# Kernel tuning notes

Hardware: AMD Instinct MI355X
Metric: run time of the kernel (lower is better)

The kernel has to match this reference:

```python
import jax, jax.numpy as jnp
import numpy as np

DIM = 64  # scaling dim from __init__


def setup_inputs() -> dict:
    key = jax.random.key(0)
    kq, kk, kv = jax.random.split(key, 3)
    B, N, D = 16, 2048, 64
    Q = jax.random.normal(kq, (B, N, D), dtype=jnp.float32)
    K = jax.random.normal(kk, (B, N, D), dtype=jnp.float32)
    V = jax.random.normal(kv, (B, N, D), dtype=jnp.float32)
    return {"Q": Q, "K": K, "V": V}


def reference(Q, K, V):
    # Original transposes K to [B, d, N]; the E/F Linformer projections are
    # constructed but their application guards are always False, so the math
    # is plain scaled-dot-product attention. Dropout p=0 (eval baseline).
    scale = 1.0 / (DIM ** 0.5)
    QK = jnp.einsum('bnd,bmd->bnm', Q, K) * scale          # [B, N, N]
    attn_weights = jax.nn.softmax(QK, axis=-1)             # [B, N, N]
    out = jnp.einsum('bnm,bmd->bnd', attn_weights, V)      # [B, N, d]
    return out, attn_weights
```

## Files before the change

### kernel.cpp

```cpp
#include <hip/hip_runtime.h>
#include <hip/hip_bf16.h>

#define B_  16
#define N_  2048
#define D_  64
#define SCALE_LOG2 0.18033688011112042f

typedef __attribute__((ext_vector_type(8))) short  frag8;
typedef __attribute__((ext_vector_type(4))) float  floatx4;

union FragU { frag8 fr; unsigned short us[8]; };

__device__ __forceinline__ unsigned short f2bf(float f) {
    return __builtin_bit_cast(unsigned short, __float2bfloat16(f));
}
__device__ __forceinline__ float exp2fast(float x) {
    return __builtin_amdgcn_exp2f(x);
}

__global__ __launch_bounds__(256) void denom_kernel(
    const float* __restrict__ Q, const float* __restrict__ K,
    float* __restrict__ ws)
{
    __shared__ unsigned short Ks[64][72];

    const int id    = blockIdx.x;
    const int xcd   = id & 7;
    const int s     = id >> 3;
    const int b     = xcd * 2 + (s >> 7);
    const int rem   = s & 127;
    const int qtile = rem >> 2;
    const int kq    = rem & 3;
    const int qbase = qtile * 64;
    const int kbase = kq * 512;
    const size_t bN = (size_t)b * N_;

    const int tid  = threadIdx.x;
    const int w    = tid >> 6;
    const int lane = tid & 63;
    const int lm   = lane & 15;
    const int quad = lane >> 4;
    const int q8   = quad * 8;
    const int srow = tid >> 2;
    const int sc0  = (tid & 3) * 16;

    FragU aq0, aq1;
    {
        const float* qp = Q + (bN + qbase + w*16 + lm) * D_;
        float4 f0 = *(const float4*)(qp + q8);
        float4 f1 = *(const float4*)(qp + q8 + 4);
        float4 f2 = *(const float4*)(qp + 32 + q8);
        float4 f3 = *(const float4*)(qp + 36 + q8);
        #pragma unroll
        for (int j = 0; j < 4; ++j) {
            aq0.us[j]   = f2bf(f0[j]);  aq0.us[4+j] = f2bf(f1[j]);
            aq1.us[j]   = f2bf(f2[j]);  aq1.us[4+j] = f2bf(f3[j]);
        }
    }

    float s4[4] = {0.f, 0.f, 0.f, 0.f};

    ushort4 kreg[4];
    {
        const float4* src = (const float4*)(K + (bN + kbase + srow) * D_ + sc0);
        #pragma unroll
        for (int i = 0; i < 4; ++i) {
            float4 f = src[i];
            kreg[i].x=f2bf(f.x); kreg[i].y=f2bf(f.y);
            kreg[i].z=f2bf(f.z); kreg[i].w=f2bf(f.w);
        }
    }

    for (int t = 0; t < 8; ++t) {
        __syncthreads();
        #pragma unroll
        for (int i = 0; i < 4; ++i)
            *(ushort4*)&Ks[srow][sc0 + i*4] = kreg[i];
        __syncthreads();

        float4 fnext[4];
        if (t + 1 < 8) {
            const float4* src = (const float4*)(K + (bN + kbase + (t+1)*64 + srow) * D_ + sc0);
            #pragma unroll
            for (int i = 0; i < 4; ++i) fnext[i] = src[i];
        }

        __builtin_amdgcn_s_setprio(1);
        #pragma unroll
        for (int ns = 0; ns < 4; ++ns) {
            frag8 b0 = *(const frag8*)&Ks[ns*16 + lm][q8];
            frag8 b1 = *(const frag8*)&Ks[ns*16 + lm][32 + q8];
            floatx4 a = {0.f, 0.f, 0.f, 0.f};
            a = __builtin_amdgcn_mfma_f32_16x16x32_bf16(aq0.fr, b0, a, 0, 0, 0);
            a = __builtin_amdgcn_mfma_f32_16x16x32_bf16(aq1.fr, b1, a, 0, 0, 0);
            #pragma unroll
            for (int r = 0; r < 4; ++r)
                s4[r] += exp2fast(a[r] * SCALE_LOG2);
        }
        __builtin_amdgcn_s_setprio(0);

        if (t + 1 < 8) {
            #pragma unroll
            for (int i = 0; i < 4; ++i) {
                kreg[i].x=f2bf(fnext[i].x); kreg[i].y=f2bf(fnext[i].y);
                kreg[i].z=f2bf(fnext[i].z); kreg[i].w=f2bf(fnext[i].w);
            }
        }
    }

    #pragma unroll
    for (int r = 0; r < 4; ++r) {
        float v = s4[r];
        #pragma unroll
        for (int off = 1; off < 16; off <<= 1)
            v += __shfl_xor(v, off, 64);
        if (lm == 0)
            atomicAdd(&ws[bN + qbase + w*16 + quad*4 + r], v);
    }
}

struct __align__(16) SMemB {
    unsigned short Ks[64][72];
    unsigned short Vt[64][72];
    float          Pf[4][16][68];
};

__global__ __launch_bounds__(256, 4) void attn_kernel(
    const float* __restrict__ Q, const float* __restrict__ K,
    const float* __restrict__ V, const float* __restrict__ ws,
    float* __restrict__ out, float* __restrict__ attn)
{
    __shared__ SMemB sm;

    const int id    = blockIdx.x;
    const int xcd   = id & 7;
    const int s     = id >> 3;
    const int b     = xcd * 2 + (s >> 6);
    const int rem   = s & 63;
    const int qtile = rem >> 1;
    const int kh    = rem & 1;
    const int qbase = qtile * 64;
    const int kbase = kh * 1024;
    const size_t bN = (size_t)b * N_;

    const int tid  = threadIdx.x;
    const int w    = tid >> 6;
    const int lane = tid & 63;
    const int lm   = lane & 15;
    const int quad = lane >> 4;
    const int q8   = quad * 8;
    const int srow = tid >> 2;
    const int sc0  = (tid & 3) * 16;
    const int vswz = srow ^ (((sc0 >> 4) & 3) << 3);

    FragU aq0, aq1;
    {
        const float* qp = Q + (bN + qbase + w*16 + lm) * D_;
        float4 f0 = *(const float4*)(qp + q8);
        float4 f1 = *(const float4*)(qp + q8 + 4);
        float4 f2 = *(const float4*)(qp + 32 + q8);
        float4 f3 = *(const float4*)(qp + 36 + q8);
        #pragma unroll
        for (int j = 0; j < 4; ++j) {
            aq0.us[j]   = f2bf(f0[j]);  aq0.us[4+j] = f2bf(f1[j]);
            aq1.us[j]   = f2bf(f2[j]);  aq1.us[4+j] = f2bf(f3[j]);
        }
    }

    float invl[4];
    #pragma unroll
    for (int r = 0; r < 4; ++r)
        invl[r] = 1.0f / ws[bN + qbase + w*16 + quad*4 + r];

    floatx4 oacc[4];
    #pragma unroll
    for (int dg = 0; dg < 4; ++dg) oacc[dg] = (floatx4){0.f, 0.f, 0.f, 0.f};

    const int prow = lane >> 3;
    const int pcol = (lane & 7) * 4;

    float4 fk[4], fv[4];
    auto loadS = [&](int t) {
        const float4* srcK = (const float4*)(K + (bN + kbase + t*64 + srow) * D_ + sc0);
        const float4* srcV = (const float4*)(V + (bN + kbase + t*64 + srow) * D_ + sc0);
        #pragma unroll
        for (int i = 0; i < 4; ++i) fk[i] = srcK[i];
        #pragma unroll
        for (int i = 0; i < 4; ++i) fv[i] = srcV[i];
    };

    loadS(0);
    for (int t = 0; t < 16; ++t) {
        __syncthreads();
        #pragma unroll
        for (int i = 0; i < 4; ++i) {
            ushort4 u; u.x=f2bf(fk[i].x); u.y=f2bf(fk[i].y);
                       u.z=f2bf(fk[i].z); u.w=f2bf(fk[i].w);
            *(ushort4*)&sm.Ks[srow][sc0 + i*4] = u;
        }
        #pragma unroll
        for (int i = 0; i < 4; ++i) {
            sm.Vt[sc0 + i*4 + 0][vswz] = f2bf(fv[i].x);
            sm.Vt[sc0 + i*4 + 1][vswz] = f2bf(fv[i].y);
            sm.Vt[sc0 + i*4 + 2][vswz] = f2bf(fv[i].z);
            sm.Vt[sc0 + i*4 + 3][vswz] = f2bf(fv[i].w);
        }
        __syncthreads();

        if (t + 1 < 16) loadS(t + 1);

        floatx4 acc[4];
        __builtin_amdgcn_s_setprio(1);
        #pragma unroll
        for (int ns = 0; ns < 4; ++ns) {
            frag8 b0 = *(const frag8*)&sm.Ks[ns*16 + lm][q8];
            frag8 b1 = *(const frag8*)&sm.Ks[ns*16 + lm][32 + q8];
            floatx4 a = {0.f, 0.f, 0.f, 0.f};
            a = __builtin_amdgcn_mfma_f32_16x16x32_bf16(aq0.fr, b0, a, 0, 0, 0);
            a = __builtin_amdgcn_mfma_f32_16x16x32_bf16(aq1.fr, b1, a, 0, 0, 0);
            acc[ns] = a;
        }
        __builtin_amdgcn_s_setprio(0);

        #pragma unroll
        for (int ns = 0; ns < 4; ++ns)
            #pragma unroll
            for (int r = 0; r < 4; ++r)
                sm.Pf[w][quad*4 + r][ns*16 + lm] =
                    exp2fast(acc[ns][r] * SCALE_LOG2) * invl[r];

        #pragma unroll
        for (int rg = 0; rg < 2; ++rg)
            #pragma unroll
            for (int half = 0; half < 2; ++half) {
                floatx4 pv = *(const floatx4*)&sm.Pf[w][rg*8 + prow][half*32 + pcol];
                __builtin_nontemporal_store(pv,
                    (floatx4*)&attn[(bN + qbase + w*16 + rg*8 + prow) * N_
                                    + kbase + t*64 + half*32 + pcol]);
            }

        FragU pa0, pa1;
        {
            float4 p0 = *(const float4*)&sm.Pf[w][lm][q8];
            float4 p1 = *(const float4*)&sm.Pf[w][lm][q8 + 4];
            float4 p2 = *(const float4*)&sm.Pf[w][lm][32 + q8];
            float4 p3 = *(const float4*)&sm.Pf[w][lm][36 + q8];
            #pragma unroll
            for (int j = 0; j < 4; ++j) {
                pa0.us[j]   = f2bf(p0[j]);  pa0.us[4+j] = f2bf(p1[j]);
                pa1.us[j]   = f2bf(p2[j]);  pa1.us[4+j] = f2bf(p3[j]);
            }
        }

        __builtin_amdgcn_s_setprio(1);
        #pragma unroll
        for (int dg = 0; dg < 4; ++dg) {
            const int kb = q8 ^ (dg << 3);
            frag8 v0 = *(const frag8*)&sm.Vt[dg*16 + lm][kb];
            frag8 v1 = *(const frag8*)&sm.Vt[dg*16 + lm][32 + kb];
            oacc[dg] = __builtin_amdgcn_mfma_f32_16x16x32_bf16(pa0.fr, v0, oacc[dg], 0, 0, 0);
            oacc[dg] = __builtin_amdgcn_mfma_f32_16x16x32_bf16(pa1.fr, v1, oacc[dg], 0, 0, 0);
        }
        __builtin_amdgcn_s_setprio(0);
    }

    #pragma unroll
    for (int dg = 0; dg < 4; ++dg)
        #pragma unroll
        for (int r = 0; r < 4; ++r)
            atomicAdd(&out[(bN + qbase + w*16 + quad*4 + r) * D_ + dg*16 + lm],
                      oacc[dg][r]);
}

extern "C" void kernel_launch(void* const* d_in, const int* in_sizes, int n_in,
                              void* d_out, int out_size, void* d_ws, size_t ws_size,
                              hipStream_t stream) {
    const float* Q = (const float*)d_in[0];
    const float* K = (const float*)d_in[1];
    const float* V = (const float*)d_in[2];
    float* out  = (float*)d_out;
    float* attn = out + (size_t)B_ * N_ * D_;
    float* ws   = (float*)d_ws;

    hipMemsetAsync(ws, 0, (size_t)B_ * N_ * sizeof(float), stream);
    hipMemsetAsync(out, 0, (size_t)B_ * N_ * D_ * sizeof(float), stream);
    denom_kernel<<<dim3(2048), 256, 0, stream>>>(Q, K, ws);
    attn_kernel <<<dim3(1024), 256, 0, stream>>>(Q, K, V, ws, out, attn);
}
```

Before: 363.1 us.

## Store unnormalized bf16 P transposed in LDS and write attn directly

Replaces the fp32 P staging buffer in shared memory with a smaller transposed bf16 buffer of unnormalized probabilities. The PV A-fragments are then gathered from it with scalar 16-bit reads, and the 1/l normalization moves to the final output atomics. Attention weights are now written straight from registers with scalar stores rather than vectorized nontemporal float4 stores through LDS. This cuts LDS footprint and traffic, but risks less efficient global store coalescing and many small LDS reads.

```diff
diff --git a/kernel.cpp b/kernel.cpp
--- a/kernel.cpp
+++ b/kernel.cpp
@@ -122,7 +122,7 @@
 struct __align__(16) SMemB {
     unsigned short Ks[64][72];
     unsigned short Vt[64][72];
-    float          Pf[4][16][68];
+    unsigned short PsT[4][64][20];
 };
 
 __global__ __launch_bounds__(256, 4) void attn_kernel(
@@ -176,9 +176,6 @@
     #pragma unroll
     for (int dg = 0; dg < 4; ++dg) oacc[dg] = (floatx4){0.f, 0.f, 0.f, 0.f};
 
-    const int prow = lane >> 3;
-    const int pcol = (lane & 7) * 4;
-
     float4 fk[4], fv[4];
     auto loadS = [&](int t) {
         const float4* srcK = (const float4*)(K + (bN + kbase + t*64 + srow) * D_ + sc0);
@@ -223,33 +220,25 @@
         __builtin_amdgcn_s_setprio(0);
 
         #pragma unroll
-        for (int ns = 0; ns < 4; ++ns)
+        for (int ns = 0; ns < 4; ++ns) {
+            float pu[4];
             #pragma unroll
             for (int r = 0; r < 4; ++r)
-                sm.Pf[w][quad*4 + r][ns*16 + lm] =
-                    exp2fast(acc[ns][r] * SCALE_LOG2) * invl[r];
-
-        #pragma unroll
-        for (int rg = 0; rg < 2; ++rg)
-            #pragma unroll
-            for (int half = 0; half < 2; ++half) {
-                floatx4 pv = *(const floatx4*)&sm.Pf[w][rg*8 + prow][half*32 + pcol];
-                __builtin_nontemporal_store(pv,
-                    (floatx4*)&attn[(bN + qbase + w*16 + rg*8 + prow) * N_
-                                    + kbase + t*64 + half*32 + pcol]);
-            }
+                pu[r] = exp2fast(acc[ns][r] * SCALE_LOG2);
+            unsigned int w0 = (unsigned int)f2bf(pu[0]) | ((unsigned int)f2bf(pu[1]) << 16);
+            unsigned int w1 = (unsigned int)f2bf(pu[2]) | ((unsigned int)f2bf(pu[3]) << 16);
+            *(uint2*)&sm.PsT[w][ns*16 + lm][quad*4] = make_uint2(w0, w1);
+            #pragma unroll
+            for (int r = 0; r < 4; ++r)
+                attn[(bN + qbase + w*16 + quad*4 + r) * N_
+                     + kbase + t*64 + ns*16 + lm] = pu[r] * invl[r];
+        }
 
         FragU pa0, pa1;
-        {
-            float4 p0 = *(const float4*)&sm.Pf[w][lm][q8];
-            float4 p1 = *(const float4*)&sm.Pf[w][lm][q8 + 4];
-            float4 p2 = *(const float4*)&sm.Pf[w][lm][32 + q8];
-            float4 p3 = *(const float4*)&sm.Pf[w][lm][36 + q8];
-            #pragma unroll
-            for (int j = 0; j < 4; ++j) {
-                pa0.us[j]   = f2bf(p0[j]);  pa0.us[4+j] = f2bf(p1[j]);
-                pa1.us[j]   = f2bf(p2[j]);  pa1.us[4+j] = f2bf(p3[j]);
-            }
+        #pragma unroll
+        for (int j = 0; j < 8; ++j) {
+            pa0.us[j] = sm.PsT[w][q8 + j][lm];
+            pa1.us[j] = sm.PsT[w][32 + q8 + j][lm];
         }
 
         __builtin_amdgcn_s_setprio(1);
@@ -269,7 +258,7 @@
         #pragma unroll
         for (int r = 0; r < 4; ++r)
             atomicAdd(&out[(bN + qbase + w*16 + quad*4 + r) * D_ + dg*16 + lm],
-                      oacc[dg][r]);
+                      oacc[dg][r] * invl[r]);
 }
 
 extern "C" void kernel_launch(void* const* d_in, const int* in_sizes, int n_in,
```

Result: no change. 366.0 us (+0.8%).
